# Optimization experiments

Measured on AMD Instinct MI355X. Metric: run time of the kernel, lower is better.

## Reference

```python
import jax, jax.numpy as jnp
import numpy as np

D_MODEL = 1024
NUM_HEADS = 16
DEPTH = D_MODEL // NUM_HEADS


def setup_inputs() -> dict:
    key = jax.random.key(0)
    ks = jax.random.split(key, 9)
    B, S = 2, 2048
    scale = 1.0 / np.sqrt(D_MODEL)
    x = jax.random.normal(ks[0], (B, S, D_MODEL), dtype=jnp.float32)
    wq = jax.random.normal(ks[1], (D_MODEL, D_MODEL), dtype=jnp.float32) * scale
    bq = jax.random.normal(ks[2], (D_MODEL,), dtype=jnp.float32) * 0.01
    wk = jax.random.normal(ks[3], (D_MODEL, D_MODEL), dtype=jnp.float32) * scale
    bk = jax.random.normal(ks[4], (D_MODEL,), dtype=jnp.float32) * 0.01
    wv = jax.random.normal(ks[5], (D_MODEL, D_MODEL), dtype=jnp.float32) * scale
    bv = jax.random.normal(ks[6], (D_MODEL,), dtype=jnp.float32) * 0.01
    wo = jax.random.normal(ks[7], (D_MODEL, D_MODEL), dtype=jnp.float32) * scale
    bo = jax.random.normal(ks[8], (D_MODEL,), dtype=jnp.float32) * 0.01
    return {"x": x, "wq": wq, "bq": bq, "wk": wk, "bk": bk,
            "wv": wv, "bv": bv, "wo": wo, "bo": bo}


def reference(x, wq, bq, wk, bk, wv, bv, wo, bo):
    B, S, _ = x.shape
    def split_heads(t):  # [B,S,D] -> [B,H,S,depth]
        return t.reshape(B, S, NUM_HEADS, DEPTH).transpose(0, 2, 1, 3)
    q = split_heads(x @ wq + bq)
    k = split_heads(x @ wk + bk)
    v = split_heads(x @ wv + bv)
    # scaled dot-product attention, full [B,H,S,S] scores as in the original
    logits = jnp.einsum('bhqd,bhkd->bhqk', q, k) / jnp.sqrt(
        jnp.asarray(DEPTH, dtype=jnp.float32))
    attn = jax.nn.softmax(logits, axis=-1)
    out = jnp.einsum('bhqk,bhkd->bhqd', attn, v)
    out = out.transpose(0, 2, 1, 3).reshape(B, S, D_MODEL)
    return out @ wo + bo
```

## Files before the change

kernel.cpp:

```cpp
#include <hip/hip_runtime.h>


#define S_LEN 2048
#define DM 1024
#define MROWS 4096
#define QSCALE 0.1803368801111244f

typedef unsigned short u16;
typedef unsigned int u32;
typedef __attribute__((ext_vector_type(8))) short short8;
typedef __attribute__((ext_vector_type(4))) float f32x4;
typedef __attribute__((ext_vector_type(4))) unsigned short u16x4;
typedef __attribute__((ext_vector_type(2))) unsigned int u32x2;

__device__ inline u16 f2bf(float f) {
    u32 u = __float_as_uint(f);
    u = u + 0x7fffu + ((u >> 16) & 1u);
    return (u16)(u >> 16);
}
__device__ inline void gld_lds16(const u16* g, u16* l) {
    __builtin_amdgcn_global_load_lds(
        (const __attribute__((address_space(1))) void*)g,
        (__attribute__((address_space(3))) void*)l, 16, 0, 0);
}
__device__ inline f32x4 mfma16(short8 a, short8 b, f32x4 c) {
    return __builtin_amdgcn_mfma_f32_16x16x32_bf16(a, b, c, 0, 0, 0);
}

__global__ void prep_all(const float* __restrict__ x, u16* __restrict__ xb,
                         const float* __restrict__ wq, const float* __restrict__ wk,
                         const float* __restrict__ wv, const float* __restrict__ wo,
                         const float* __restrict__ bq, const float* __restrict__ bk,
                         const float* __restrict__ bv, const float* __restrict__ bo,
                         u16* __restrict__ wallT, u16* __restrict__ woT,
                         float* __restrict__ biasAll, float* __restrict__ biasO) {
    const int t = threadIdx.x;
    if (blockIdx.x < 2048) {
        const size_t i8 = ((size_t)blockIdx.x * 256 + t) * 8;
        const f32x4 a = ((const f32x4*)x)[i8 / 4];
        const f32x4 b = ((const f32x4*)x)[i8 / 4 + 1];
        u16 o[8];
#pragma unroll
        for (int i = 0; i < 4; i++) { o[i] = f2bf(a[i]); o[4 + i] = f2bf(b[i]); }
        *(short8*)(xb + i8) = *(const short8*)o;
        return;
    }
    const int bid = blockIdx.x - 2048;
    if (bid == 1024) {
#pragma unroll
        for (int i = 0; i < 4; i++) {
            const int idx = i * 256 + t;
            biasAll[idx]        = bq[idx] * QSCALE;
            biasAll[1024 + idx] = bk[idx];
            biasAll[2048 + idx] = bv[idx];
            biasO[idx]          = bo[idx];
        }
        return;
    }
    __shared__ float lds[64][65];
    const int m  = bid >> 8;
    const int tk = (bid >> 4) & 15;
    const int tn = bid & 15;
    const float* src = (m == 0) ? wq : (m == 1) ? wk : (m == 2) ? wv : wo;
    const float scale = (m == 0) ? QSCALE : 1.0f;
    const int r4 = t >> 6, c = t & 63;
#pragma unroll
    for (int i = 0; i < 16; i++) {
        const int k = tk * 64 + i * 4 + r4;
        lds[i * 4 + r4][c] = src[(size_t)k * 1024 + tn * 64 + c];
    }
    __syncthreads();
#pragma unroll
    for (int i = 0; i < 16; i++) {
        const int n = tn * 64 + i * 4 + r4;
        const int k = tk * 64 + c;
        const u16 v = f2bf(lds[c][i * 4 + r4] * scale);
        if (m < 3) wallT[((size_t)m * 1024 + n) * 1024 + k] = v;
        else       woT[(size_t)n * 1024 + k] = v;
    }
}

__global__ __launch_bounds__(256, 2)
void gemm_qkv(const u16* __restrict__ A, const u16* __restrict__ Bt,
              const float* __restrict__ bias, u16* __restrict__ Cq,
              u16* __restrict__ Ck, u16* __restrict__ Cv,
              const int K, const int N) {
    __shared__ __align__(16) u16 As[128 * 32];
    __shared__ __align__(16) u16 Bs[128 * 32];
    __shared__ __align__(16) u16 Ct[128 * 136];
    const int tid = threadIdx.x;
    const int w = tid >> 6, lane = tid & 63;
    const int wm = w >> 1, wn = w & 1;
    const int l16 = lane & 15, quad = lane >> 4;
    const int tm = blockIdx.x * 128;
    const int tn = blockIdx.y * 128;
    const int region = tn >> 10;

    const int sr = w * 16 + (lane >> 2);
    const int sc = (lane & 3) * 8;
    const u16* ag0 = A + (size_t)(tm + sr) * K + sc;
    const u16* ag1 = A + (size_t)(tm + sr + 64) * K + sc;
    const u16* bg0 = Bt + (size_t)(tn + sr) * K + sc;
    const u16* bg1 = Bt + (size_t)(tn + sr + 64) * K + sc;
    u16* al = As + w * 512;
    u16* bl = Bs + w * 512;

    f32x4 acc[4][4];
#pragma unroll
    for (int i = 0; i < 4; i++)
#pragma unroll
        for (int j = 0; j < 4; j++) acc[i][j] = (f32x4){0.f, 0.f, 0.f, 0.f};

    for (int kb = 0; kb < K; kb += 32) {
        __syncthreads();
        gld_lds16(ag0 + kb, al);
        gld_lds16(ag1 + kb, al + 2048);
        gld_lds16(bg0 + kb, bl);
        gld_lds16(bg1 + kb, bl + 2048);
        __syncthreads();
        short8 af[4], bfr[4];
#pragma unroll
        for (int i = 0; i < 4; i++) {
            af[i]  = *(const short8*)(As + (wm * 64 + i * 16 + l16) * 32 + quad * 8);
            bfr[i] = *(const short8*)(Bs + (wn * 64 + i * 16 + l16) * 32 + quad * 8);
        }
#pragma unroll
        for (int i = 0; i < 4; i++)
#pragma unroll
            for (int j = 0; j < 4; j++)
                acc[i][j] = mfma16(af[i], bfr[j], acc[i][j]);
    }

    if (region < 2) {
#pragma unroll
        for (int j = 0; j < 4; j++) {
            const int colL = wn * 64 + j * 16 + l16;
            const float bv = bias[tn + colL];
#pragma unroll
            for (int i = 0; i < 4; i++) {
                const int row0 = wm * 64 + i * 16 + quad * 4;
#pragma unroll
                for (int r = 0; r < 4; r++)
                    Ct[(row0 + r) * 136 + colL] = f2bf(acc[i][j][r] + bv);
            }
        }
    } else {
#pragma unroll
        for (int j = 0; j < 4; j++) {
            const int colL = wn * 64 + j * 16 + l16;
            const float bv = bias[tn + colL];
#pragma unroll
            for (int i = 0; i < 4; i++) {
                const int row0 = wm * 64 + i * 16 + quad * 4;
                u16x4 pk;
#pragma unroll
                for (int r = 0; r < 4; r++) pk[r] = f2bf(acc[i][j][r] + bv);
                *(u16x4*)(Ct + colL * 132 + row0) = pk;
            }
        }
    }
    __syncthreads();

    if (region == 0) {
#pragma unroll
        for (int p = 0; p < 8; p++) {
            const int rowL = p * 16 + (tid >> 4);
            const int c8 = (tid & 15) * 8;
            const short8 v = *(const short8*)(Ct + rowL * 136 + c8);
            *(short8*)(Cq + (size_t)(tm + rowL) * 1024 + tn + c8) = v;
        }
    } else if (region == 1) {
        const int b = tm >> 11, sBase = tm & 2047;
#pragma unroll
        for (int p = 0; p < 8; p++) {
            const int rowL = p * 16 + (tid >> 4);
            const int c8 = (tid & 15) * 8;
            const short8 v = *(const short8*)(Ct + rowL * 136 + c8);
            const int s = sBase + rowL;
            const int hd = (tn - 1024) + c8;
            const int h = hd >> 6, dd = hd & 63;
            const int chunk = ((dd >> 3) + s) & 7;
            *(short8*)(Ck + (((size_t)(b * 16 + h) * 2048 + s) << 6) + chunk * 8) = v;
        }
    } else {
        const int b = tm >> 11, tBase = (tm & 2047) >> 6;
        const int hBase = (tn >> 6) - 32;
#pragma unroll
        for (int p = 0; p < 8; p++) {
            const int cid = p * 256 + tid;
            const int q3 = cid & 7;
            const int colL = (cid >> 3) & 127;
            const int half = cid >> 10;
            const int d = colL & 63;
            const int h = hBase + (colL >> 6);
            const int c = (q3 - d) & 7;
            const int base = (c & 3) * 4 + ((c & 4) << 3);
            const u32x2 Ar = *(const u32x2*)(Ct + colL * 132 + half * 64 + base);
            const u32x2 Br = *(const u32x2*)(Ct + colL * 132 + half * 64 + base + 16);
            union { u32 u[4]; short8 s8; } o;
            o.u[0] = __builtin_amdgcn_perm(Br[0], Ar[0], 0x05040100u);
            o.u[1] = __builtin_amdgcn_perm(Br[0], Ar[0], 0x07060302u);
            o.u[2] = __builtin_amdgcn_perm(Br[1], Ar[1], 0x05040100u);
            o.u[3] = __builtin_amdgcn_perm(Br[1], Ar[1], 0x07060302u);
            *(short8*)(Cv + (((size_t)((b * 16 + h) * 32 + tBase + half)) << 12) +
                       d * 64 + q3 * 8) = o.s8;
        }
    }
}

__global__ __launch_bounds__(256, 2)
void gemm_out64(const u16* __restrict__ A, const u16* __restrict__ Bt,
                const float* __restrict__ bias, float* __restrict__ C,
                const int K, const int N) {
    __shared__ __align__(16) u16 As[64 * 32];
    __shared__ __align__(16) u16 Bs[128 * 32];
    const int tid = threadIdx.x;
    const int w = tid >> 6, lane = tid & 63;
    const int wm = w >> 1, wn = w & 1;
    const int l16 = lane & 15, quad = lane >> 4;
    const int tm = blockIdx.x * 64;
    const int tn = blockIdx.y * 128;

    const int sr = w * 16 + (lane >> 2);
    const int sc = (lane & 3) * 8;
    const u16* ag  = A + (size_t)(tm + sr) * K + sc;
    const u16* bg0 = Bt + (size_t)(tn + sr) * K + sc;
    const u16* bg1 = Bt + (size_t)(tn + sr + 64) * K + sc;
    u16* al = As + w * 512;
    u16* bl = Bs + w * 512;

    f32x4 acc[2][4];
#pragma unroll
    for (int i = 0; i < 2; i++)
#pragma unroll
        for (int j = 0; j < 4; j++) acc[i][j] = (f32x4){0.f, 0.f, 0.f, 0.f};

    for (int kb = 0; kb < K; kb += 32) {
        __syncthreads();
        gld_lds16(ag + kb, al);
        gld_lds16(bg0 + kb, bl);
        gld_lds16(bg1 + kb, bl + 2048);
        __syncthreads();
        short8 af[2], bfr[4];
#pragma unroll
        for (int i = 0; i < 2; i++)
            af[i] = *(const short8*)(As + (wm * 32 + i * 16 + l16) * 32 + quad * 8);
#pragma unroll
        for (int j = 0; j < 4; j++)
            bfr[j] = *(const short8*)(Bs + (wn * 64 + j * 16 + l16) * 32 + quad * 8);
#pragma unroll
        for (int i = 0; i < 2; i++)
#pragma unroll
            for (int j = 0; j < 4; j++)
                acc[i][j] = mfma16(af[i], bfr[j], acc[i][j]);
    }
#pragma unroll
    for (int j = 0; j < 4; j++) {
        const int col = tn + wn * 64 + j * 16 + l16;
        const float bv = bias[col];
#pragma unroll
        for (int i = 0; i < 2; i++) {
            const int row0 = tm + wm * 32 + i * 16 + quad * 4;
#pragma unroll
            for (int r = 0; r < 4; r++)
                C[(size_t)(row0 + r) * N + col] = acc[i][j][r] + bv;
        }
    }
}

__global__ __launch_bounds__(256, 2)
void flash_attn(const u16* __restrict__ Qb, const u16* __restrict__ Ktg,
                const u16* __restrict__ Vtb, u16* __restrict__ O) {
    __shared__ __align__(16) u16 SB[4][8192];
    __shared__ float osumS[4][4][16];
    const int tid = threadIdx.x;
    const int w = tid >> 6, lane = tid & 63;
    const int l16 = lane & 15, quad = lane >> 4;
    const int bh = blockIdx.y, b = bh >> 4, h = bh & 15;
    const int qg = w >> 1, kh = w & 1;
    const int q0 = blockIdx.x * 128 + qg * 64;

    short8 qf[4][2];
#pragma unroll
    for (int u = 0; u < 4; u++) {
        const size_t qrow = (size_t)(b * S_LEN + q0 + u * 16 + l16) * 1024 + h * 64;
        qf[u][0] = *(const short8*)(Qb + qrow + quad * 8);
        qf[u][1] = *(const short8*)(Qb + qrow + 32 + quad * 8);
    }
    u16 ones_s[8];
#pragma unroll
    for (int i = 0; i < 8; i++) ones_s[i] = 0x3F80u;
    const short8 ones = *(const short8*)ones_s;

    const u16* kg = Ktg + ((size_t)bh << 17) + ((size_t)kh << 16) + lane * 8;
    const u16* vg = Vtb + ((size_t)bh << 17) + ((size_t)kh << 16) + lane * 8;
    u16* kl = &SB[w][0];
    u16* vl = &SB[w][4096];

    const int ka0 = l16 * 64 + ((quad + l16) & 7) * 8;
    const int ka1 = l16 * 64 + ((4 + quad + l16) & 7) * 8;

    f32x4 o[4][4], osum[4];
#pragma unroll
    for (int u = 0; u < 4; u++) {
        osum[u] = (f32x4){0.f, 0.f, 0.f, 0.f};
#pragma unroll
        for (int d = 0; d < 4; d++) o[u][d] = (f32x4){0.f, 0.f, 0.f, 0.f};
    }
    const f32x4 zz = (f32x4){0.f, 0.f, 0.f, 0.f};

    for (int t = 0; t < 16; t++) {
        __builtin_amdgcn_sched_barrier(0);
        const int off = t * 4096;
#pragma unroll
        for (int j = 0; j < 8; j++) gld_lds16(kg + off + j * 512, kl + j * 512);
#pragma unroll
        for (int j = 0; j < 8; j++) gld_lds16(vg + off + j * 512, vl + j * 512);
        __builtin_amdgcn_s_waitcnt(0x0F70);
        __builtin_amdgcn_sched_barrier(0);

        f32x4 s[4][4];
#pragma unroll
        for (int a = 0; a < 4; a++) {
            const short8 kf0 = *(const short8*)(kl + a * 1024 + ka0);
            const short8 kf1 = *(const short8*)(kl + a * 1024 + ka1);
#pragma unroll
            for (int u = 0; u < 4; u++) {
                s[u][a] = mfma16(kf0, qf[u][0], zz);
                s[u][a] = mfma16(kf1, qf[u][1], s[u][a]);
            }
        }
        union { u32 u[4]; short8 s8; } pu[4][2];
#pragma unroll
        for (int u = 0; u < 4; u++) {
#pragma unroll
            for (int r = 0; r < 4; r++) {
                const float e0 = __builtin_amdgcn_exp2f(s[u][0][r]);
                const float e1 = __builtin_amdgcn_exp2f(s[u][1][r]);
                const float e2 = __builtin_amdgcn_exp2f(s[u][2][r]);
                const float e3 = __builtin_amdgcn_exp2f(s[u][3][r]);
                pu[u][0].u[r] = __builtin_amdgcn_perm(
                    __float_as_uint(e1), __float_as_uint(e0), 0x07060302u);
                pu[u][1].u[r] = __builtin_amdgcn_perm(
                    __float_as_uint(e3), __float_as_uint(e2), 0x07060302u);
            }
            osum[u] = mfma16(ones, pu[u][0].s8, osum[u]);
            osum[u] = mfma16(ones, pu[u][1].s8, osum[u]);
        }
#pragma unroll
        for (int dv = 0; dv < 4; dv++) {
            const short8 vf0 = *(const short8*)(vl + dv * 1024 + ka0);
            const short8 vf1 = *(const short8*)(vl + dv * 1024 + ka1);
#pragma unroll
            for (int u = 0; u < 4; u++) {
                o[u][dv] = mfma16(vf0, pu[u][0].s8, o[u][dv]);
                o[u][dv] = mfma16(vf1, pu[u][1].s8, o[u][dv]);
            }
        }
    }

    float* pb = (float*)&SB[w][0];
#pragma unroll
    for (int u = 0; u < 4; u++) {
#pragma unroll
        for (int dv = 0; dv < 4; dv++)
            *(f32x4*)(pb + (u * 4 + dv) * 256 + lane * 4) = o[u][dv];
        if (quad == 0) osumS[w][u][l16] = osum[u][0];
    }
    __syncthreads();
    if (kh == 0) {
        const float* qb2 = (const float*)&SB[w + 1][0];
#pragma unroll
        for (int u = 0; u < 4; u++) {
            const float inv = 1.0f / (osumS[w][u][l16] + osumS[w + 1][u][l16]);
            const size_t obase =
                (size_t)(b * S_LEN + q0 + u * 16 + l16) * DM + h * 64 + quad * 4;
#pragma unroll
            for (int dv = 0; dv < 4; dv++) {
                const f32x4 other = *(const f32x4*)(qb2 + (u * 4 + dv) * 256 + lane * 4);
                u16x4 pk;
#pragma unroll
                for (int r = 0; r < 4; r++)
                    pk[r] = f2bf((o[u][dv][r] + other[r]) * inv);
                *(u16x4*)(O + obase + dv * 16) = pk;
            }
        }
    }
}

extern "C" void kernel_launch(void* const* d_in, const int* in_sizes, int n_in,
                              void* d_out, int out_size, void* d_ws, size_t ws_size,
                              hipStream_t stream) {
    const float* x  = (const float*)d_in[0];
    const float* wq = (const float*)d_in[1];
    const float* bq = (const float*)d_in[2];
    const float* wk = (const float*)d_in[3];
    const float* bk = (const float*)d_in[4];
    const float* wv = (const float*)d_in[5];
    const float* bv = (const float*)d_in[6];
    const float* wo = (const float*)d_in[7];
    const float* bo = (const float*)d_in[8];

    char* ws = (char*)d_ws;
    u16*   wallT   = (u16*)(ws + 64);
    u16*   woT     = (u16*)(ws + 6291520);
    float* biasAll = (float*)(ws + 8388672);
    float* biasO   = (float*)(ws + 8400960);
    u16*   xb      = (u16*)(ws + 8405056);
    u16*   Qb      = (u16*)(ws + 16793664);
    u16*   Ktg     = (u16*)(ws + 25182272);
    u16*   Vtb     = (u16*)(ws + 33570880);
    u16*   Obuf    = (u16*)(ws + 41959488);

    prep_all<<<3073, 256, 0, stream>>>(x, xb, wq, wk, wv, wo, bq, bk, bv, bo,
                                       wallT, woT, biasAll, biasO);
    gemm_qkv<<<dim3(32, 24), 256, 0, stream>>>(xb, wallT, biasAll,
                                               Qb, Ktg, Vtb, 1024, 3072);
    flash_attn<<<dim3(16, 32), 256, 0, stream>>>(Qb, Ktg, Vtb, Obuf);
    gemm_out64<<<dim3(64, 8), 256, 0, stream>>>(Obuf, woT, biasO,
                                                (float*)d_out, 1024, 1024);
}
```

Measured before the change: 183.6 us.

## Split flash attention keys four ways per block and load K/V directly to registers

The attention kernel now processes 64 queries per block with all four waves sharing those queries, each wave covering a quarter of the keys. The final reduction combines four partial outputs and denominators through shared memory, and the grid grows to four times as many blocks. K and V tiles are read straight from global memory into registers instead of being staged through LDS with global_load_lds and waitcnt. This targets low occupancy and LDS staging overhead, at the cost of more redundant Q loads, a larger cross-wave reduction, and loads whose latency is now hidden only by the compiler's scheduling of the unrolled loop.

```diff
diff --git a/kernel.cpp b/kernel.cpp
--- a/kernel.cpp
+++ b/kernel.cpp
@@ -271,14 +271,13 @@
 __global__ __launch_bounds__(256, 2)
 void flash_attn(const u16* __restrict__ Qb, const u16* __restrict__ Ktg,
                 const u16* __restrict__ Vtb, u16* __restrict__ O) {
-    __shared__ __align__(16) u16 SB[4][8192];
-    __shared__ float osumS[4][4][16];
+    __shared__ f32x4 PB[3][16][64];
+    __shared__ float OS[3][4][16];
     const int tid = threadIdx.x;
     const int w = tid >> 6, lane = tid & 63;
     const int l16 = lane & 15, quad = lane >> 4;
     const int bh = blockIdx.y, b = bh >> 4, h = bh & 15;
-    const int qg = w >> 1, kh = w & 1;
-    const int q0 = blockIdx.x * 128 + qg * 64;
+    const int q0 = blockIdx.x * 64;
 
     short8 qf[4][2];
 #pragma unroll
@@ -292,11 +291,8 @@
     for (int i = 0; i < 8; i++) ones_s[i] = 0x3F80u;
     const short8 ones = *(const short8*)ones_s;
 
-    const u16* kg = Ktg + ((size_t)bh << 17) + ((size_t)kh << 16) + lane * 8;
-    const u16* vg = Vtb + ((size_t)bh << 17) + ((size_t)kh << 16) + lane * 8;
-    u16* kl = &SB[w][0];
-    u16* vl = &SB[w][4096];
-
+    const u16* kq = Ktg + ((size_t)bh << 17) + ((size_t)w << 15);
+    const u16* vq = Vtb + ((size_t)bh << 17) + ((size_t)w << 15);
     const int ka0 = l16 * 64 + ((quad + l16) & 7) * 8;
     const int ka1 = l16 * 64 + ((4 + quad + l16) & 7) * 8;
 
@@ -309,25 +305,28 @@
     }
     const f32x4 zz = (f32x4){0.f, 0.f, 0.f, 0.f};
 
-    for (int t = 0; t < 16; t++) {
-        __builtin_amdgcn_sched_barrier(0);
-        const int off = t * 4096;
-#pragma unroll
-        for (int j = 0; j < 8; j++) gld_lds16(kg + off + j * 512, kl + j * 512);
-#pragma unroll
-        for (int j = 0; j < 8; j++) gld_lds16(vg + off + j * 512, vl + j * 512);
-        __builtin_amdgcn_s_waitcnt(0x0F70);
-        __builtin_amdgcn_sched_barrier(0);
-
+#pragma unroll
+    for (int t = 0; t < 8; t++) {
+        const u16* kt = kq + t * 4096;
+        const u16* vt = vq + t * 4096;
+        short8 kf[4][2], vf[4][2];
+#pragma unroll
+        for (int a = 0; a < 4; a++) {
+            kf[a][0] = *(const short8*)(kt + a * 1024 + ka0);
+            kf[a][1] = *(const short8*)(kt + a * 1024 + ka1);
+        }
+#pragma unroll
+        for (int dv = 0; dv < 4; dv++) {
+            vf[dv][0] = *(const short8*)(vt + dv * 1024 + ka0);
+            vf[dv][1] = *(const short8*)(vt + dv * 1024 + ka1);
+        }
         f32x4 s[4][4];
 #pragma unroll
         for (int a = 0; a < 4; a++) {
-            const short8 kf0 = *(const short8*)(kl + a * 1024 + ka0);
-            const short8 kf1 = *(const short8*)(kl + a * 1024 + ka1);
 #pragma unroll
             for (int u = 0; u < 4; u++) {
-                s[u][a] = mfma16(kf0, qf[u][0], zz);
-                s[u][a] = mfma16(kf1, qf[u][1], s[u][a]);
+                s[u][a] = mfma16(kf[a][0], qf[u][0], zz);
+                s[u][a] = mfma16(kf[a][1], qf[u][1], s[u][a]);
             }
         }
         union { u32 u[4]; short8 s8; } pu[4][2];
@@ -349,39 +348,41 @@
         }
 #pragma unroll
         for (int dv = 0; dv < 4; dv++) {
-            const short8 vf0 = *(const short8*)(vl + dv * 1024 + ka0);
-            const short8 vf1 = *(const short8*)(vl + dv * 1024 + ka1);
 #pragma unroll
             for (int u = 0; u < 4; u++) {
-                o[u][dv] = mfma16(vf0, pu[u][0].s8, o[u][dv]);
-                o[u][dv] = mfma16(vf1, pu[u][1].s8, o[u][dv]);
-            }
-        }
-    }
-
-    float* pb = (float*)&SB[w][0];
-#pragma unroll
-    for (int u = 0; u < 4; u++) {
-#pragma unroll
-        for (int dv = 0; dv < 4; dv++)
-            *(f32x4*)(pb + (u * 4 + dv) * 256 + lane * 4) = o[u][dv];
-        if (quad == 0) osumS[w][u][l16] = osum[u][0];
+                o[u][dv] = mfma16(vf[dv][0], pu[u][0].s8, o[u][dv]);
+                o[u][dv] = mfma16(vf[dv][1], pu[u][1].s8, o[u][dv]);
+            }
+        }
+    }
+
+    if (w > 0) {
+#pragma unroll
+        for (int u = 0; u < 4; u++) {
+#pragma unroll
+            for (int dv = 0; dv < 4; dv++)
+                PB[w - 1][u * 4 + dv][lane] = o[u][dv];
+            if (quad == 0) OS[w - 1][u][l16] = osum[u][0];
+        }
     }
     __syncthreads();
-    if (kh == 0) {
-        const float* qb2 = (const float*)&SB[w + 1][0];
+    if (w == 0) {
 #pragma unroll
         for (int u = 0; u < 4; u++) {
-            const float inv = 1.0f / (osumS[w][u][l16] + osumS[w + 1][u][l16]);
+            const float den = osum[u][0] + OS[0][u][l16] + OS[1][u][l16] +
+                              OS[2][u][l16];
+            const float inv = 1.0f / den;
             const size_t obase =
                 (size_t)(b * S_LEN + q0 + u * 16 + l16) * DM + h * 64 + quad * 4;
 #pragma unroll
             for (int dv = 0; dv < 4; dv++) {
-                const f32x4 other = *(const f32x4*)(qb2 + (u * 4 + dv) * 256 + lane * 4);
+                const f32x4 p0 = PB[0][u * 4 + dv][lane];
+                const f32x4 p1 = PB[1][u * 4 + dv][lane];
+                const f32x4 p2 = PB[2][u * 4 + dv][lane];
                 u16x4 pk;
 #pragma unroll
                 for (int r = 0; r < 4; r++)
-                    pk[r] = f2bf((o[u][dv][r] + other[r]) * inv);
+                    pk[r] = f2bf((o[u][dv][r] + p0[r] + p1[r] + p2[r]) * inv);
                 *(u16x4*)(O + obase + dv * 16) = pk;
             }
         }
@@ -416,7 +417,7 @@
                                        wallT, woT, biasAll, biasO);
     gemm_qkv<<<dim3(32, 24), 256, 0, stream>>>(xb, wallT, biasAll,
                                                Qb, Ktg, Vtb, 1024, 3072);
-    flash_attn<<<dim3(16, 32), 256, 0, stream>>>(Qb, Ktg, Vtb, Obuf);
+    flash_attn<<<dim3(64, 32), 256, 0, stream>>>(Qb, Ktg, Vtb, Obuf);
     gemm_out64<<<dim3(64, 8), 256, 0, stream>>>(Obuf, woT, biasO,
                                                 (float*)d_out, 1024, 1024);
 }
```

Measured after the change: 239.6 us. 30.5% more time.

## Share K/V tiles across query-group waves in LDS and reorder block mapping

Applied to the files above, without the earlier changes.

Flash attention now has the two waves that process the same key half share one K/V tile in LDS. Each wave loads a quarter of the tile and block-wide barriers replace per-wave waitcnt, which halves global K/V traffic per block and cuts LDS from 64KB to 32KB. Blocks are remapped so consecutive block IDs cover different batch-heads at the same query offset. The gemm_qkv launch bounds are raised to three blocks per SIMD. The cost is two __syncthreads per iteration, which can stall waves, and the register cap on the GEMM may cause spills.

```diff
diff --git a/kernel.cpp b/kernel.cpp
--- a/kernel.cpp
+++ b/kernel.cpp
@@ -80,7 +80,7 @@
     }
 }
 
-__global__ __launch_bounds__(256, 2)
+__global__ __launch_bounds__(256, 3)
 void gemm_qkv(const u16* __restrict__ A, const u16* __restrict__ Bt,
               const float* __restrict__ bias, u16* __restrict__ Cq,
               u16* __restrict__ Ck, u16* __restrict__ Cv,
@@ -271,14 +271,16 @@
 __global__ __launch_bounds__(256, 2)
 void flash_attn(const u16* __restrict__ Qb, const u16* __restrict__ Ktg,
                 const u16* __restrict__ Vtb, u16* __restrict__ O) {
-    __shared__ __align__(16) u16 SB[4][8192];
-    __shared__ float osumS[4][4][16];
+    __shared__ __align__(16) u16 Ks[2][4096];
+    __shared__ __align__(16) u16 Vs[2][4096];
+    __shared__ float OS[2][4][16];
     const int tid = threadIdx.x;
     const int w = tid >> 6, lane = tid & 63;
     const int l16 = lane & 15, quad = lane >> 4;
-    const int bh = blockIdx.y, b = bh >> 4, h = bh & 15;
-    const int qg = w >> 1, kh = w & 1;
-    const int q0 = blockIdx.x * 128 + qg * 64;
+    const int lid = blockIdx.x + blockIdx.y * 16;
+    const int bh = lid & 31, b = bh >> 4, h = bh & 15;
+    const int qg = w & 1, kh = w >> 1;
+    const int q0 = (lid >> 5) * 128 + qg * 64;
 
     short8 qf[4][2];
 #pragma unroll
@@ -292,10 +294,10 @@
     for (int i = 0; i < 8; i++) ones_s[i] = 0x3F80u;
     const short8 ones = *(const short8*)ones_s;
 
-    const u16* kg = Ktg + ((size_t)bh << 17) + ((size_t)kh << 16) + lane * 8;
-    const u16* vg = Vtb + ((size_t)bh << 17) + ((size_t)kh << 16) + lane * 8;
-    u16* kl = &SB[w][0];
-    u16* vl = &SB[w][4096];
+    const u16* kg = Ktg + ((size_t)bh << 17) + ((size_t)kh << 16) + qg * 2048 + lane * 8;
+    const u16* vg = Vtb + ((size_t)bh << 17) + ((size_t)kh << 16) + qg * 2048 + lane * 8;
+    u16* kl = Ks[kh] + qg * 2048;
+    u16* vl = Vs[kh] + qg * 2048;
 
     const int ka0 = l16 * 64 + ((quad + l16) & 7) * 8;
     const int ka1 = l16 * 64 + ((4 + quad + l16) & 7) * 8;
@@ -310,20 +312,23 @@
     const f32x4 zz = (f32x4){0.f, 0.f, 0.f, 0.f};
 
     for (int t = 0; t < 16; t++) {
-        __builtin_amdgcn_sched_barrier(0);
+        __syncthreads();
         const int off = t * 4096;
-#pragma unroll
-        for (int j = 0; j < 8; j++) gld_lds16(kg + off + j * 512, kl + j * 512);
-#pragma unroll
-        for (int j = 0; j < 8; j++) gld_lds16(vg + off + j * 512, vl + j * 512);
-        __builtin_amdgcn_s_waitcnt(0x0F70);
-        __builtin_amdgcn_sched_barrier(0);
+        gld_lds16(kg + off,        kl);
+        gld_lds16(kg + off + 512,  kl + 512);
+        gld_lds16(kg + off + 1024, kl + 1024);
+        gld_lds16(kg + off + 1536, kl + 1536);
+        gld_lds16(vg + off,        vl);
+        gld_lds16(vg + off + 512,  vl + 512);
+        gld_lds16(vg + off + 1024, vl + 1024);
+        gld_lds16(vg + off + 1536, vl + 1536);
+        __syncthreads();
 
         f32x4 s[4][4];
 #pragma unroll
         for (int a = 0; a < 4; a++) {
-            const short8 kf0 = *(const short8*)(kl + a * 1024 + ka0);
-            const short8 kf1 = *(const short8*)(kl + a * 1024 + ka1);
+            const short8 kf0 = *(const short8*)(Ks[kh] + a * 1024 + ka0);
+            const short8 kf1 = *(const short8*)(Ks[kh] + a * 1024 + ka1);
 #pragma unroll
             for (int u = 0; u < 4; u++) {
                 s[u][a] = mfma16(kf0, qf[u][0], zz);
@@ -349,8 +354,8 @@
         }
 #pragma unroll
         for (int dv = 0; dv < 4; dv++) {
-            const short8 vf0 = *(const short8*)(vl + dv * 1024 + ka0);
-            const short8 vf1 = *(const short8*)(vl + dv * 1024 + ka1);
+            const short8 vf0 = *(const short8*)(Vs[kh] + dv * 1024 + ka0);
+            const short8 vf1 = *(const short8*)(Vs[kh] + dv * 1024 + ka1);
 #pragma unroll
             for (int u = 0; u < 4; u++) {
                 o[u][dv] = mfma16(vf0, pu[u][0].s8, o[u][dv]);
@@ -359,25 +364,28 @@
         }
     }
 
-    float* pb = (float*)&SB[w][0];
-#pragma unroll
-    for (int u = 0; u < 4; u++) {
-#pragma unroll
-        for (int dv = 0; dv < 4; dv++)
-            *(f32x4*)(pb + (u * 4 + dv) * 256 + lane * 4) = o[u][dv];
-        if (quad == 0) osumS[w][u][l16] = osum[u][0];
+    __syncthreads();
+    if (kh == 1) {
+        float* pb = (qg == 0) ? (float*)&Ks[0][0] : (float*)&Vs[0][0];
+#pragma unroll
+        for (int u = 0; u < 4; u++) {
+#pragma unroll
+            for (int dv = 0; dv < 4; dv++)
+                *(f32x4*)(pb + (u * 4 + dv) * 256 + lane * 4) = o[u][dv];
+            if (quad == 0) OS[qg][u][l16] = osum[u][0];
+        }
     }
     __syncthreads();
     if (kh == 0) {
-        const float* qb2 = (const float*)&SB[w + 1][0];
+        const float* pb = (qg == 0) ? (const float*)&Ks[0][0] : (const float*)&Vs[0][0];
 #pragma unroll
         for (int u = 0; u < 4; u++) {
-            const float inv = 1.0f / (osumS[w][u][l16] + osumS[w + 1][u][l16]);
+            const float inv = 1.0f / (osum[u][0] + OS[qg][u][l16]);
             const size_t obase =
                 (size_t)(b * S_LEN + q0 + u * 16 + l16) * DM + h * 64 + quad * 4;
 #pragma unroll
             for (int dv = 0; dv < 4; dv++) {
-                const f32x4 other = *(const f32x4*)(qb2 + (u * 4 + dv) * 256 + lane * 4);
+                const f32x4 other = *(const f32x4*)(pb + (u * 4 + dv) * 256 + lane * 4);
                 u16x4 pk;
 #pragma unroll
                 for (int r = 0; r < 4; r++)
```

Result: no change. 183.2 us (-0.3%).
